# Kernel tuning notes

Hardware: AMD Instinct MI355X
Metric: run time of the kernel (lower is better)

The kernel has to match this reference:

```python
import jax, jax.numpy as jnp
import numpy as np
from jax import lax

B, S, I, H, O = 64, 512, 512, 1024, 2


def setup_inputs() -> dict:
    key = jax.random.key(0)
    ks = jax.random.split(key, 16)
    sc = 0.02
    def w(k, shape):
        return jax.random.normal(k, shape, dtype=jnp.float32) * sc
    inp = {
        "x": jax.random.normal(ks[0], (B, S, I), dtype=jnp.float32),
        # layer 0 GRU gates: Linear(I+H, H)
        "Wr0": w(ks[1], (H, I + H)), "br0": jnp.zeros((H,), jnp.float32),
        "Wz0": w(ks[2], (H, I + H)), "bz0": jnp.zeros((H,), jnp.float32),
        "Wc0": w(ks[3], (H, I + H)), "bc0": jnp.zeros((H,), jnp.float32),
        # layer 1 GRU gates: Linear(H+H, H)
        "Wr1": w(ks[4], (H, 2 * H)), "br1": jnp.zeros((H,), jnp.float32),
        "Wz1": w(ks[5], (H, 2 * H)), "bz1": jnp.zeros((H,), jnp.float32),
        "Wc1": w(ks[6], (H, 2 * H)), "bc1": jnp.zeros((H,), jnp.float32),
        "Wreg": w(ks[7], (O, H)), "breg": jnp.zeros((O,), jnp.float32),
    }
    return inp


def _gru_cell(h, xin, Wr, br, Wz, bz, Wc, bc):
    # Faithful to source GRUCell: note h*z + (1-z)*can (inverted vs standard GRU).
    xh = jnp.concatenate([xin, h], axis=1)
    r = jax.nn.sigmoid(xh @ Wr.T + br)
    z = jax.nn.sigmoid(xh @ Wz.T + bz)
    can = jnp.tanh(jnp.concatenate([xin, h * r], axis=1) @ Wc.T + bc)
    return h * z + (1.0 - z) * can


def reference(x, Wr0, br0, Wz0, bz0, Wc0, bc0, Wr1, br1, Wz1, bz1, Wc1, bc1, Wreg, breg):
    b = x.shape[0]
    hdim = Wr0.shape[0]
    h0_init = jnp.zeros((b, hdim), x.dtype)
    h1_init = jnp.zeros((b, hdim), x.dtype)

    def step(carry, xt):
        h0, h1 = carry
        h0 = _gru_cell(h0, xt, Wr0, br0, Wz0, bz0, Wc0, bc0)
        h1 = _gru_cell(h1, h0, Wr1, br1, Wz1, bz1, Wc1, bc1)
        return (h0, h1), None

    xs = jnp.swapaxes(x, 0, 1)  # [S, B, I]
    (h0, h1), _ = lax.scan(step, (h0_init, h1_init), xs)
    return h1 @ Wreg.T + breg
```

## Files before the change

### kernel.cpp

```cpp
#include <hip/hip_runtime.h>


typedef _Float16 f16;
typedef f16  f16x8 __attribute__((ext_vector_type(8)));
typedef float f32x4 __attribute__((ext_vector_type(4)));
typedef unsigned long long u64;

#define NB   64
#define SEQ  512
#define IDIM 512
#define HDIM 1024
#define NBH  (NB*HDIM)

#define OFF_H0   0u
#define OFF_H1   262144u
#define OFF_H0R  524288u
#define OFF_H1R  655360u
#define OFF_BAR  786432u
#define OFF_W16  790528u
#define W16_L0_ELEMS 4718592u

#define SMEM_BYTES 37888

__device__ __forceinline__ float sigf(float x){ return 1.0f/(1.0f+__expf(-x)); }
__device__ __forceinline__ float tanh_fast(float x){ float e=__expf(2.0f*x); return 1.0f - 2.0f/(e+1.0f); }

__device__ __forceinline__ f16x8 cload16(const f16* p){
  f16x8 r;
  asm volatile("global_load_dwordx4 %0, %1, off sc0 sc1" : "=v"(r) : "v"(p));
  return r;
}
__device__ __forceinline__ void cstore8(f16* p, u64 v){
  asm volatile("global_store_dwordx2 %0, %1, off sc0 sc1" :: "v"(p), "v"(v) : "memory");
}

__device__ __forceinline__ f16x8 load_x_frag(const float* p){
  f32x4 v0 = *(const f32x4*)p;
  f32x4 v1 = *(const f32x4*)(p+4);
  f16x8 r;
  r[0]=(f16)v0[0]; r[1]=(f16)v0[1]; r[2]=(f16)v0[2]; r[3]=(f16)v0[3];
  r[4]=(f16)v1[0]; r[5]=(f16)v1[1]; r[6]=(f16)v1[2]; r[7]=(f16)v1[3];
  return r;
}

__device__ __forceinline__ void group_barrier(char* gb, unsigned& lgen){
  asm volatile("s_waitcnt vmcnt(0) lgkmcnt(0)" ::: "memory");
  __syncthreads();
  if (threadIdx.x == 0){
    unsigned* cnt = (unsigned*)gb;
    unsigned* gen = (unsigned*)(gb + 256);
    const unsigned tgt = lgen + 1u;
    unsigned old = __hip_atomic_fetch_add(cnt, 1u, __ATOMIC_RELAXED, __HIP_MEMORY_SCOPE_AGENT);
    if (old == tgt*64u - 1u){
      __hip_atomic_store(gen, tgt, __ATOMIC_RELAXED, __HIP_MEMORY_SCOPE_AGENT);
    }
    while (__hip_atomic_load(gen, __ATOMIC_RELAXED, __HIP_MEMORY_SCOPE_AGENT) < tgt){
      __builtin_amdgcn_s_sleep(2);
    }
    lgen = tgt;
  }
  __syncthreads();
}

template<int LAYER>
__device__ void run_rnn(int g, int n32, const float* x,
    const float* brp, const float* bzp, const float* bcp,
    char* ws, char* smem, char* gb){
  constexpr int K   = (LAYER==0) ? 1536 : 2048;
  constexpr int NKS = K/32;
  constexpr int KW  = NKS/8;
  const int tid  = threadIdx.x;
  const int lane = tid & 63;
  const int kg   = tid >> 6;
  const int quad = lane >> 4;
  const int qo   = quad*8;
  const int m_base = g*16;
  const int n_base = n32*32;
  const int arow   = m_base + (lane & 15);

  f32x4* red = (f32x4*)smem;
  float* zst = (float*)(smem + 32768);
  f16*   hst = (f16*)  (smem + 34816);
  float* hf  = (float*)(smem + 35840);

  hf[tid & 511] = 0.f;
  __syncthreads();

  f16* h0m = (f16*)(ws + OFF_H0);
  f16* h1m = (f16*)(ws + OFF_H1);
  f16* h0r = (f16*)(ws + OFF_H0R);
  f16* h1r = (f16*)(ws + OFF_H1R);
  f16* hrbuf = (LAYER==0)? h0r : h1r;
  f16* hown  = (LAYER==0)? h0m : h1m;
  const char* w16L = ws + OFF_W16 + (LAYER ? (size_t)W16_L0_ELEMS*2 : 0);

  const size_t lo = (size_t)lane*16;
  const int nt0 = n32*2, nt1 = n32*2 + 1;
  const char* bR0 = w16L + ((size_t)((0*64 + nt0)*NKS + kg*KW))*1024 + lo;
  const char* bR1 = w16L + ((size_t)((0*64 + nt1)*NKS + kg*KW))*1024 + lo;
  const char* bZ0 = w16L + ((size_t)((1*64 + nt0)*NKS + kg*KW))*1024 + lo;
  const char* bZ1 = w16L + ((size_t)((1*64 + nt1)*NKS + kg*KW))*1024 + lo;
  const char* bC0 = w16L + ((size_t)((2*64 + nt0)*NKS + kg*KW))*1024 + lo;
  const char* bC1 = w16L + ((size_t)((2*64 + nt1)*NKS + kg*KW))*1024 + lo;

  const int col_own = n_base + (kg & 1)*16 + (lane & 15);
  const float bRv = brp[col_own], bZv = bzp[col_own], bCv = bcp[col_own];

  unsigned lgen = 0;
  f16x8 fa[KW];

  for (int iter = 0; iter <= SEQ; ++iter){
    const int  t    = (LAYER==0) ? iter : (iter-1);
    const bool act  = (LAYER==0) ? (iter < SEQ) : (iter >= 1);
    const int  bufA = (iter & 1) ^ 1;

    if (act){
#pragma unroll
      for (int j=0;j<KW;++j){
        int ks = kg*KW + j;
        if (LAYER==0){
          if (ks < 16)
            fa[j] = load_x_frag(x + ((size_t)arow*SEQ + t)*IDIM + ks*32 + qo);
          else
            fa[j] = cload16(h0m + (size_t)bufA*NBH + (size_t)arow*HDIM + (ks-16)*32 + qo);
        } else {
          if (ks < 32)
            fa[j] = cload16(h0m + (size_t)bufA*NBH + (size_t)arow*HDIM + ks*32 + qo);
          else
            fa[j] = cload16(h1m + (size_t)(iter&1)*NBH + (size_t)arow*HDIM + (ks-32)*32 + qo);
        }
      }
      asm volatile("s_waitcnt vmcnt(0)" ::: "memory");
      f32x4 aR0{0,0,0,0}, aR1{0,0,0,0}, aZ0{0,0,0,0}, aZ1{0,0,0,0};
#pragma unroll
      for (int j=0;j<KW;++j){
        aR0 = __builtin_amdgcn_mfma_f32_16x16x32_f16(fa[j], *(const f16x8*)(bR0 + j*1024), aR0,0,0,0);
        aR1 = __builtin_amdgcn_mfma_f32_16x16x32_f16(fa[j], *(const f16x8*)(bR1 + j*1024), aR1,0,0,0);
        aZ0 = __builtin_amdgcn_mfma_f32_16x16x32_f16(fa[j], *(const f16x8*)(bZ0 + j*1024), aZ0,0,0,0);
        aZ1 = __builtin_amdgcn_mfma_f32_16x16x32_f16(fa[j], *(const f16x8*)(bZ1 + j*1024), aZ1,0,0,0);
      }
      red[(0*8+kg)*64+lane] = aR0;  red[(1*8+kg)*64+lane] = aR1;
      red[(2*8+kg)*64+lane] = aZ0;  red[(3*8+kg)*64+lane] = aZ1;
    }
    __syncthreads();
    if (act && kg < 4){
      f32x4 s = red[(kg*8+0)*64+lane];
#pragma unroll
      for (int k2=1;k2<8;++k2) s += red[(kg*8+k2)*64+lane];
      const int coll = (kg&1)*16 + (lane&15);
#pragma unroll
      for (int i=0;i<4;++i){
        int rowl = quad*4 + i;
        if (kg < 2){
          float r = sigf(s[i] + bRv);
          hst[rowl*32 + coll] = (f16)(hf[rowl*32+coll] * r);
        } else {
          zst[rowl*32 + coll] = sigf(s[i] + bZv);
        }
      }
    }
    __syncthreads();
    if (act && tid < 128){
      int rowl = tid>>3, c8 = (tid&7)*4;
      u64 v = *(const u64*)(hst + rowl*32 + c8);
      cstore8(hrbuf + (size_t)(m_base+rowl)*HDIM + n_base + c8, v);
    }
    group_barrier(gb, lgen);

    if (act){
#pragma unroll
      for (int j=0;j<KW;++j){
        int ks = kg*KW + j;
        if (LAYER==0){
          if (ks >= 16)
            fa[j] = cload16(h0r + (size_t)arow*HDIM + (ks-16)*32 + qo);
        } else {
          if (ks >= 32)
            fa[j] = cload16(h1r + (size_t)arow*HDIM + (ks-32)*32 + qo);
        }
      }
      asm volatile("s_waitcnt vmcnt(0)" ::: "memory");
      f32x4 aC0{0,0,0,0}, aC1{0,0,0,0};
#pragma unroll
      for (int j=0;j<KW;++j){
        aC0 = __builtin_amdgcn_mfma_f32_16x16x32_f16(fa[j], *(const f16x8*)(bC0 + j*1024), aC0,0,0,0);
        aC1 = __builtin_amdgcn_mfma_f32_16x16x32_f16(fa[j], *(const f16x8*)(bC1 + j*1024), aC1,0,0,0);
      }
      red[(0*8+kg)*64+lane] = aC0;  red[(1*8+kg)*64+lane] = aC1;
    }
    __syncthreads();
    if (act && kg < 2){
      f32x4 s = red[(kg*8+0)*64+lane];
#pragma unroll
      for (int k2=1;k2<8;++k2) s += red[(kg*8+k2)*64+lane];
      const int coll = kg*16 + (lane&15);
#pragma unroll
      for (int i=0;i<4;++i){
        int rowl = quad*4 + i;
        float can = tanh_fast(s[i] + bCv);
        float z   = zst[rowl*32 + coll];
        float hnew = hf[rowl*32+coll]*z + (1.0f - z)*can;
        hf[rowl*32+coll]  = hnew;
        hst[rowl*32+coll] = (f16)hnew;
      }
    }
    __syncthreads();
    if (act && tid < 128){
      const int bufW = (LAYER==0) ? (iter&1) : ((iter&1)^1);
      int rowl = tid>>3, c8 = (tid&7)*4;
      u64 v = *(const u64*)(hst + rowl*32 + c8);
      cstore8(hown + (size_t)bufW*NBH + (size_t)(m_base+rowl)*HDIM + n_base + c8, v);
    }
    group_barrier(gb, lgen);
  }
}

__global__ void __launch_bounds__(512, 2)
rnn_kernel(const float* x,
           const float* br0, const float* bz0, const float* bc0,
           const float* br1, const float* bz1, const float* bc1,
           const float* Wreg, const float* breg,
           float* out, char* ws){
  extern __shared__ char smem[];
  const int b = blockIdx.x;
  const int xcd = b & 7, slot = b >> 3;
  const int g = slot & 3, phi = slot >> 2;
  const int p = phi*8 + xcd;
  const int layer = p >> 5, n32 = p & 31;
  char* gb = ws + OFF_BAR + (size_t)g*1024;

  if (layer==0) run_rnn<0>(g, n32, x, br0,bz0,bc0, ws, smem, gb);
  else          run_rnn<1>(g, n32, x, br1,bz1,bc1, ws, smem, gb);

  if (layer==1 && n32==0 && threadIdx.x < 32){
    int mrow = g*16 + ((int)threadIdx.x >> 1), o = threadIdx.x & 1;
    const f16* hp = (const f16*)(ws + OFF_H1) + (size_t)NBH + (size_t)mrow*HDIM;
    const float* wp = Wreg + (size_t)o*HDIM;
    float acc = 0.f;
#pragma unroll 4
    for (int k=0;k<HDIM;k+=4){
      u64 q = __hip_atomic_load((const u64*)(hp+k), __ATOMIC_RELAXED, __HIP_MEMORY_SCOPE_AGENT);
      union { u64 qq; f16 h[4]; } u; u.qq = q;
      acc += (float)u.h[0]*wp[k]   + (float)u.h[1]*wp[k+1]
           + (float)u.h[2]*wp[k+2] + (float)u.h[3]*wp[k+3];
    }
    out[mrow*2 + o] = acc + breg[o];
  }
}

__global__ void prep_w(const float* Wr0, const float* Wz0, const float* Wc0,
                       const float* Wr1, const float* Wz1, const float* Wc1,
                       f16* w16){
  size_t i = (size_t)blockIdx.x*256 + threadIdx.x;
  const bool l1 = (i >= (size_t)W16_L0_ELEMS);
  size_t j = l1 ? i - (size_t)W16_L0_ELEMS : i;
  const int K   = l1 ? 2048 : 1536;
  const int NKS = K >> 5;
  int e    = (int)(j & 7);
  int lane = (int)((j >> 3) & 63);
  size_t r = j >> 9;
  int ks   = (int)(r % (size_t)NKS);
  size_t gnt = r / (size_t)NKS;
  int nt   = (int)(gnt & 63);
  int gate = (int)(gnt >> 6);
  int n = nt*16 + (lane & 15);
  int k = ks*32 + ((lane >> 4) << 3) + e;
  const float* W = l1 ? (gate==0 ? Wr1 : gate==1 ? Wz1 : Wc1)
                      : (gate==0 ? Wr0 : gate==1 ? Wz0 : Wc0);
  w16[i] = (f16)W[(size_t)n*K + k];
}

extern "C" void kernel_launch(void* const* d_in, const int* in_sizes, int n_in,
                              void* d_out, int out_size, void* d_ws, size_t ws_size,
                              hipStream_t stream){
  const float* x    = (const float*)d_in[0];
  const float* Wr0  = (const float*)d_in[1];
  const float* br0  = (const float*)d_in[2];
  const float* Wz0  = (const float*)d_in[3];
  const float* bz0  = (const float*)d_in[4];
  const float* Wc0  = (const float*)d_in[5];
  const float* bc0  = (const float*)d_in[6];
  const float* Wr1  = (const float*)d_in[7];
  const float* br1  = (const float*)d_in[8];
  const float* Wz1  = (const float*)d_in[9];
  const float* bz1  = (const float*)d_in[10];
  const float* Wc1  = (const float*)d_in[11];
  const float* bc1  = (const float*)d_in[12];
  const float* Wreg = (const float*)d_in[13];
  const float* breg = (const float*)d_in[14];
  float* out = (float*)d_out;
  char*  ws  = (char*)d_ws;

  hipMemsetAsync(ws, 0, OFF_W16, stream);

  prep_w<<<43008, 256, 0, stream>>>(Wr0, Wz0, Wc0, Wr1, Wz1, Wc1,
                                    (f16*)(ws + OFF_W16));

  hipFuncSetAttribute((const void*)rnn_kernel,
                      hipFuncAttributeMaxDynamicSharedMemorySize, 160*1024);

  void* args[] = { (void*)&x,
                   (void*)&br0, (void*)&bz0, (void*)&bc0,
                   (void*)&br1, (void*)&bz1, (void*)&bc1,
                   (void*)&Wreg, (void*)&breg,
                   (void*)&out, (void*)&ws };
  hipLaunchCooperativeKernel((const void*)rnn_kernel, dim3(256), dim3(512),
                             args, (unsigned)SMEM_BYTES, stream);
}
```

Measured before the change: 6.416 ms.

## Replace group-wide atomic barrier with per-block progress flags and targeted waits

The single counter-based barrier shared by all 64 blocks of a batch group is replaced by per-block monotonic progress flags, one per phase and layer. Each block waits only on the specific producer flags it depends on (layer-0 phase flags, layer-1 phase flags), with 64 lanes polling the 32 flags in parallel. This removes the contended fetch-add and lets the two layers drift in a loosely pipelined way instead of marching in lockstep. The cost is more polling traffic, and the ordering of hidden-state buffers across layers must stay correct under the relaxed dependencies.

```diff
diff --git a/kernel.cpp b/kernel.cpp
--- a/kernel.cpp
+++ b/kernel.cpp
@@ -17,7 +17,7 @@
 #define OFF_H0R  524288u
 #define OFF_H1R  655360u
 #define OFF_BAR  786432u
-#define OFF_W16  790528u
+#define OFF_W16  794624u
 #define W16_L0_ELEMS 4718592u
 
 #define SMEM_BYTES 37888
@@ -43,21 +43,15 @@
   return r;
 }
 
-__device__ __forceinline__ void group_barrier(char* gb, unsigned& lgen){
-  asm volatile("s_waitcnt vmcnt(0) lgkmcnt(0)" ::: "memory");
-  __syncthreads();
-  if (threadIdx.x == 0){
-    unsigned* cnt = (unsigned*)gb;
-    unsigned* gen = (unsigned*)(gb + 256);
-    const unsigned tgt = lgen + 1u;
-    unsigned old = __hip_atomic_fetch_add(cnt, 1u, __ATOMIC_RELAXED, __HIP_MEMORY_SCOPE_AGENT);
-    if (old == tgt*64u - 1u){
-      __hip_atomic_store(gen, tgt, __ATOMIC_RELAXED, __HIP_MEMORY_SCOPE_AGENT);
-    }
-    while (__hip_atomic_load(gen, __ATOMIC_RELAXED, __HIP_MEMORY_SCOPE_AGENT) < tgt){
-      __builtin_amdgcn_s_sleep(2);
-    }
-    lgen = tgt;
+__device__ __forceinline__ void wait2(const unsigned* f0, unsigned t0,
+                                      const unsigned* f1, unsigned t1){
+  if (threadIdx.x < 64){
+    const int l = threadIdx.x;
+    const unsigned* p = (l < 32) ? (f0 + l) : (f1 + (l - 32));
+    const unsigned tgt = (l < 32) ? t0 : t1;
+    while (__hip_atomic_load(p, __ATOMIC_RELAXED, __HIP_MEMORY_SCOPE_AGENT) < tgt){
+      __builtin_amdgcn_s_sleep(1);
+    }
   }
   __syncthreads();
 }
@@ -65,7 +59,7 @@
 template<int LAYER>
 __device__ void run_rnn(int g, int n32, const float* x,
     const float* brp, const float* bzp, const float* bcp,
-    char* ws, char* smem, char* gb){
+    char* ws, char* smem, unsigned* fl){
   constexpr int K   = (LAYER==0) ? 1536 : 2048;
   constexpr int NKS = K/32;
   constexpr int KW  = NKS/8;
@@ -78,6 +72,9 @@
   const int n_base = n32*32;
   const int arow   = m_base + (lane & 15);
 
+  unsigned* myA = fl + (LAYER ? 128 : 0);
+  unsigned* myB = fl + (LAYER ? 192 : 64);
+
   f32x4* red = (f32x4*)smem;
   float* zst = (float*)(smem + 32768);
   f16*   hst = (f16*)  (smem + 34816);
@@ -106,13 +103,16 @@
   const int col_own = n_base + (kg & 1)*16 + (lane & 15);
   const float bRv = brp[col_own], bZv = bzp[col_own], bCv = bcp[col_own];
 
-  unsigned lgen = 0;
   f16x8 fa[KW];
 
   for (int iter = 0; iter <= SEQ; ++iter){
     const int  t    = (LAYER==0) ? iter : (iter-1);
     const bool act  = (LAYER==0) ? (iter < SEQ) : (iter >= 1);
     const int  bufA = (iter & 1) ^ 1;
+    const unsigned ui = (unsigned)iter;
+
+    if (LAYER==0) wait2(fl+64, ui, fl+64, ui);
+    else          wait2(fl+64, ui, fl+192, ui);
 
     if (act){
 #pragma unroll
@@ -165,7 +165,13 @@
       u64 v = *(const u64*)(hst + rowl*32 + c8);
       cstore8(hrbuf + (size_t)(m_base+rowl)*HDIM + n_base + c8, v);
     }
-    group_barrier(gb, lgen);
+    asm volatile("s_waitcnt vmcnt(0)" ::: "memory");
+    __syncthreads();
+    if (tid == 0)
+      __hip_atomic_store(myA + n32, ui + 1u, __ATOMIC_RELAXED, __HIP_MEMORY_SCOPE_AGENT);
+
+    if (LAYER==0) wait2(fl+0,   ui+1u, fl+128, ui);
+    else          wait2(fl+128, ui+1u, fl+128, ui+1u);
 
     if (act){
 #pragma unroll
@@ -211,7 +217,10 @@
       u64 v = *(const u64*)(hst + rowl*32 + c8);
       cstore8(hown + (size_t)bufW*NBH + (size_t)(m_base+rowl)*HDIM + n_base + c8, v);
     }
-    group_barrier(gb, lgen);
+    asm volatile("s_waitcnt vmcnt(0)" ::: "memory");
+    __syncthreads();
+    if (tid == 0)
+      __hip_atomic_store(myB + n32, ui + 1u, __ATOMIC_RELAXED, __HIP_MEMORY_SCOPE_AGENT);
   }
 }
 
@@ -227,24 +236,27 @@
   const int g = slot & 3, phi = slot >> 2;
   const int p = phi*8 + xcd;
   const int layer = p >> 5, n32 = p & 31;
-  char* gb = ws + OFF_BAR + (size_t)g*1024;
-
-  if (layer==0) run_rnn<0>(g, n32, x, br0,bz0,bc0, ws, smem, gb);
-  else          run_rnn<1>(g, n32, x, br1,bz1,bc1, ws, smem, gb);
-
-  if (layer==1 && n32==0 && threadIdx.x < 32){
-    int mrow = g*16 + ((int)threadIdx.x >> 1), o = threadIdx.x & 1;
-    const f16* hp = (const f16*)(ws + OFF_H1) + (size_t)NBH + (size_t)mrow*HDIM;
-    const float* wp = Wreg + (size_t)o*HDIM;
-    float acc = 0.f;
+  unsigned* fl = (unsigned*)(ws + OFF_BAR + (size_t)g*2048);
+
+  if (layer==0) run_rnn<0>(g, n32, x, br0,bz0,bc0, ws, smem, fl);
+  else          run_rnn<1>(g, n32, x, br1,bz1,bc1, ws, smem, fl);
+
+  if (layer==1 && n32==0){
+    wait2(fl+192, (unsigned)SEQ + 1u, fl+192, (unsigned)SEQ + 1u);
+    if (threadIdx.x < 32){
+      int mrow = g*16 + ((int)threadIdx.x >> 1), o = threadIdx.x & 1;
+      const f16* hp = (const f16*)(ws + OFF_H1) + (size_t)NBH + (size_t)mrow*HDIM;
+      const float* wp = Wreg + (size_t)o*HDIM;
+      float acc = 0.f;
 #pragma unroll 4
-    for (int k=0;k<HDIM;k+=4){
-      u64 q = __hip_atomic_load((const u64*)(hp+k), __ATOMIC_RELAXED, __HIP_MEMORY_SCOPE_AGENT);
-      union { u64 qq; f16 h[4]; } u; u.qq = q;
-      acc += (float)u.h[0]*wp[k]   + (float)u.h[1]*wp[k+1]
-           + (float)u.h[2]*wp[k+2] + (float)u.h[3]*wp[k+3];
-    }
-    out[mrow*2 + o] = acc + breg[o];
+      for (int k=0;k<HDIM;k+=4){
+        u64 q = __hip_atomic_load((const u64*)(hp+k), __ATOMIC_RELAXED, __HIP_MEMORY_SCOPE_AGENT);
+        union { u64 qq; f16 h[4]; } u; u.qq = q;
+        acc += (float)u.h[0]*wp[k]   + (float)u.h[1]*wp[k+1]
+             + (float)u.h[2]*wp[k+2] + (float)u.h[3]*wp[k+3];
+      }
+      out[mrow*2 + o] = acc + breg[o];
+    }
   }
 }
 
```

New measurement: 6.968 ms. 1.09x slower.
